# Kernel optimization log

Hardware: AMD Instinct MI355X
Metric: run time of the kernel (lower is better)

## Reference

```python
import jax, jax.numpy as jnp
import numpy as np

B, S, E = 8, 4096, 128
H, O = 64, 64  # attention_hidden_dim, out_dim


def setup_inputs() -> dict:
    key = jax.random.key(0)
    ks = jax.random.split(key, 4)
    x = jax.random.normal(ks[0], (B, S, E), dtype=jnp.float32)
    Wq = jax.random.normal(ks[1], (E, H), dtype=jnp.float32) * (1.0 / np.sqrt(E))
    Wk = jax.random.normal(ks[2], (E, H), dtype=jnp.float32) * (1.0 / np.sqrt(E))
    Wv = jax.random.normal(ks[3], (E, O), dtype=jnp.float32) * (1.0 / np.sqrt(E))
    bq = jnp.zeros((H,), dtype=jnp.float32)
    bk = jnp.zeros((H,), dtype=jnp.float32)
    bv = jnp.zeros((O,), dtype=jnp.float32)
    return {"x": x, "Wq": Wq, "bq": bq, "Wk": Wk, "bk": bk, "Wv": Wv, "bv": bv}


def reference(x, Wq, bq, Wk, bk, Wv, bv):
    # Batched version of the per-sample loop: q = x@Wq+bq, etc.
    q = jnp.einsum("bse,eh->bsh", x, Wq) + bq   # [B,S,H]
    k = jnp.einsum("bse,eh->bsh", x, Wk) + bk   # [B,S,H]
    v = jnp.einsum("bse,eo->bso", x, Wv) + bv   # [B,S,O]
    scores = jnp.einsum("bqh,bkh->bqk", q, k)   # QK^T per sample, [B,S,S]
    attn = jax.nn.softmax(scores, axis=-1)       # softmax over key dim
    out = jnp.einsum("bqk,bko->bqo", attn, v)   # [B,S,O]
    return out
```

## Files before the change

kernel.cpp:

```cpp
#include <hip/hip_runtime.h>
#include <math.h>

#define BB 8
#define SS 4096
#define EE 128
#define HH 64
#define NT 16
#define LOG2E 1.44269504088896f

typedef _Float16 f16;
typedef __attribute__((ext_vector_type(8))) _Float16 f16x8;
typedef __attribute__((ext_vector_type(4))) float f32x4;

__device__ __forceinline__ unsigned int pk2h(float a, float b) {
    return __builtin_bit_cast(unsigned int, __builtin_amdgcn_cvt_pkrtz(a, b));
}

__device__ __forceinline__ void async_copy16(void* lds, const void* g) {
    __builtin_amdgcn_global_load_lds(
        (const __attribute__((address_space(1))) void*)g,
        (__attribute__((address_space(3))) void*)lds, 16, 0, 0);
}

__device__ __forceinline__ void vm_barrier() {
    asm volatile("s_waitcnt vmcnt(0) lgkmcnt(0)" ::: "memory");
    __builtin_amdgcn_s_barrier();
    __builtin_amdgcn_sched_barrier(0);
}

__global__ __launch_bounds__(256) void wtrans_kernel(
    const float* __restrict__ Wq, const float* __restrict__ Wk,
    const float* __restrict__ Wv, f16* __restrict__ Wt)
{
    const int idx = blockIdx.x * 256 + threadIdx.x;
    if (idx >= 192 * 128) return;
    const int col = idx >> 7, e = idx & 127;
    const float v = (col < 64)  ? Wq[e * 64 + col] * LOG2E
                  : (col < 128) ? Wk[e * 64 + (col - 64)]
                                : Wv[e * 64 + (col - 128)];
    Wt[col * 128 + e] = (f16)v;
}

__global__ __launch_bounds__(256) void qkv_kernel(
    const float* __restrict__ x, const f16* __restrict__ Wt,
    const float* __restrict__ bq, const float* __restrict__ bk,
    const float* __restrict__ bv,
    f16* __restrict__ Q, f16* __restrict__ K, f16* __restrict__ Vt)
{
    __shared__ __align__(16) short xs[64 * EE];
    const int tid = threadIdx.x;
    const long rowbase = (long)blockIdx.x * 64;

    {
        const float4* xg = (const float4*)(x + rowbase * EE);
#pragma unroll
        for (int j = 0; j < 8; ++j) {
            const int eidx = tid * 32 + j * 4;
            const float4 v = xg[eidx >> 2];
            unsigned long long pk =
                (unsigned long long)pk2h(v.x, v.y) |
                ((unsigned long long)pk2h(v.z, v.w) << 32);
            const int row = eidx >> 7;
            const int off = (row * 256 + (eidx & 127) * 2) ^ ((row & 7) << 4);
            *(unsigned long long*)((char*)xs + off) = pk;
        }
    }
    __syncthreads();

    const int lane = tid & 63;
    const int wid  = tid >> 6;
    const int ln15 = lane & 15;
    const int lg   = lane >> 4;

    f16x8 xa[4];
    {
        const int row = wid * 16 + ln15;
        const int swz = (row & 7) << 4;
#pragma unroll
        for (int s = 0; s < 4; ++s)
            xa[s] = *(const f16x8*)((const char*)xs + ((row * 256 + lg * 16 + s * 64) ^ swz));
    }

    f32x4 acc[12];
#pragma unroll
    for (int ct = 0; ct < 12; ++ct) acc[ct] = (f32x4){0.f, 0.f, 0.f, 0.f};

#pragma unroll
    for (int ct = 0; ct < 12; ++ct) {
        const f16* wtp = Wt + (ct * 16 + ln15) * 128 + lg * 8;
#pragma unroll
        for (int s = 0; s < 4; ++s) {
            const f16x8 wb = *(const f16x8*)(wtp + s * 32);
            acc[ct] = __builtin_amdgcn_mfma_f32_16x16x32_f16(xa[s], wb, acc[ct], 0, 0, 0);
        }
    }

    const long grow0 = rowbase + wid * 16 + 4 * lg;
#pragma unroll
    for (int ct = 0; ct < 4; ++ct) {
        const int col = ct * 16 + ln15;
        const float b = bq[col] * LOG2E;
#pragma unroll
        for (int r = 0; r < 4; ++r)
            Q[(grow0 + r) * HH + col] = (f16)(acc[ct][r] + b);
    }
#pragma unroll
    for (int ct = 4; ct < 8; ++ct) {
        const int col = (ct - 4) * 16 + ln15;
        const float b = bk[col];
#pragma unroll
        for (int r = 0; r < 4; ++r)
            K[(grow0 + r) * HH + col] = (f16)(acc[ct][r] + b);
    }
    {
        const long batch = rowbase >> 12;
        const long inrow = (rowbase & 4095) + wid * 16 + 4 * lg;
#pragma unroll
        for (int ct = 8; ct < 12; ++ct) {
            const int o = (ct - 8) * 16 + ln15;
            const float b = bv[o];
            unsigned long long pk =
                (unsigned long long)pk2h(acc[ct][0] + b, acc[ct][1] + b) |
                ((unsigned long long)pk2h(acc[ct][2] + b, acc[ct][3] + b) << 32);
            *(unsigned long long*)(Vt + ((long)batch * HH + o) * SS + inrow) = pk;
        }
    }
}

__global__ __launch_bounds__(256, 4) void flash_kernel(
    const f16* __restrict__ Q, const f16* __restrict__ K,
    const f16* __restrict__ Vt, f16* __restrict__ Onorm,
    float* __restrict__ lse)
{
    __shared__ __align__(16) short k_s[2][64 * HH];
    __shared__ __align__(16) short v_s[2][64 * HH];
    __shared__ __align__(16) short p_s[4 * 16 * HH];

    const int tid  = threadIdx.x;
    const int lane = tid & 63;
    const int wid  = tid >> 6;
    const int ln15 = lane & 15;
    const int lg   = lane >> 4;
    const int batch = blockIdx.x & 7;
    const int rest  = blockIdx.x >> 3;
    const int split = rest & 3;
    const int qtile = rest >> 2;
    const int k0base = split * (SS / 4);

    f16x8 qf[2];
    {
        const long qrow = (long)batch * SS + qtile * 64 + wid * 16 + ln15;
        const f16* qp = Q + qrow * HH + lg * 8;
        qf[0] = *(const f16x8*)(qp);
        qf[1] = *(const f16x8*)(qp + 32);
    }

    f32x4 oacc[4];
#pragma unroll
    for (int ot = 0; ot < 4; ++ot) oacc[ot] = (f32x4){0.f, 0.f, 0.f, 0.f};
    float m = -1e30f, l = 0.f;

    short* pw = p_s + wid * (16 * HH);
    const int swq = (ln15 & 7) << 4;

    const int crow = lane >> 3;
    const int ccs  = ((lane & 7) * 16) ^ (crow << 4);
    const int row0 = wid * 16 + crow;
    const char* kgb = (const char*)(K + ((long)batch * SS + k0base) * HH);
    const char* vgb = (const char*)(Vt + (long)batch * HH * SS);
    const long koff = (long)row0 * 128 + ccs;
    const long voff = (long)row0 * (SS * 2) + k0base * 2 + ccs;

    auto issue = [&](int t, int b) __attribute__((always_inline)) {
        char* kl = (char*)k_s[b] + wid * 2048;
        char* vl = (char*)v_s[b] + wid * 2048;
        const char* kg = kgb + (long)t * (64 * 128) + koff;
        const char* vg = vgb + (long)t * 128 + voff;
        async_copy16(kl,        kg);
        async_copy16(kl + 1024, kg + 1024);
        async_copy16(vl,        vg);
        async_copy16(vl + 1024, vg + 8 * (SS * 2));
    };

    auto compute = [&](int cur) __attribute__((always_inline)) {
        const short* ks = k_s[cur];
        const short* vs = v_s[cur];

        f32x4 sacc[4];
        __builtin_amdgcn_s_setprio(1);
#pragma unroll
        for (int kt = 0; kt < 4; ++kt) {
            f32x4 a = (f32x4){0.f, 0.f, 0.f, 0.f};
            const int key = kt * 16 + ln15;
            const int rb = key * 128, swz = (key & 7) << 4;
            const f16x8 ka0 = *(const f16x8*)((const char*)ks + ((rb + lg * 16) ^ swz));
            const f16x8 ka1 = *(const f16x8*)((const char*)ks + ((rb + lg * 16 + 64) ^ swz));
            a = __builtin_amdgcn_mfma_f32_16x16x32_f16(ka0, qf[0], a, 0, 0, 0);
            a = __builtin_amdgcn_mfma_f32_16x16x32_f16(ka1, qf[1], a, 0, 0, 0);
            sacc[kt] = a;
        }
        __builtin_amdgcn_s_setprio(0);

        float t0 = fmaxf(fmaxf(sacc[0][0], sacc[0][1]), sacc[0][2]);
        float t1 = fmaxf(fmaxf(sacc[0][3], sacc[1][0]), sacc[1][1]);
        float t2 = fmaxf(fmaxf(sacc[1][2], sacc[1][3]), sacc[2][0]);
        float t3 = fmaxf(fmaxf(sacc[2][1], sacc[2][2]), sacc[2][3]);
        float t4 = fmaxf(fmaxf(sacc[3][0], sacc[3][1]), sacc[3][2]);
        float tm = fmaxf(fmaxf(fmaxf(t0, t1), t2), fmaxf(fmaxf(t3, t4), sacc[3][3]));
        tm = fmaxf(tm, __shfl_xor(tm, 16));
        tm = fmaxf(tm, __shfl_xor(tm, 32));
        if (!__all(tm <= m + 11.5f)) {
            const float mn = fmaxf(m, tm);
            const float alpha = __builtin_amdgcn_exp2f(m - mn);
            l *= alpha;
#pragma unroll
            for (int r = 0; r < 4; ++r) {
                const float ar = __shfl(alpha, lg * 4 + r);
                oacc[0][r] *= ar; oacc[1][r] *= ar;
                oacc[2][r] *= ar; oacc[3][r] *= ar;
            }
            m = mn;
        }

        float ps = 0.f;
#pragma unroll
        for (int kt = 0; kt < 4; ++kt)
#pragma unroll
            for (int r = 0; r < 4; ++r) {
                const float pv = __builtin_amdgcn_exp2f(sacc[kt][r] - m);
                sacc[kt][r] = pv;
                ps += pv;
            }
        ps += __shfl_xor(ps, 16);
        ps += __shfl_xor(ps, 32);
        l += ps;

#pragma unroll
        for (int kt = 0; kt < 4; ++kt) {
            uint2 pk;
            pk.x = pk2h(sacc[kt][0], sacc[kt][1]);
            pk.y = pk2h(sacc[kt][2], sacc[kt][3]);
            const int key = kt * 16 + lg * 4;
            *(uint2*)((char*)pw + ((ln15 * 128 + key * 2) ^ swq)) = pk;
        }

        __builtin_amdgcn_s_setprio(1);
#pragma unroll
        for (int s = 0; s < 2; ++s) {
            const f16x8 pa = *(const f16x8*)((const char*)pw + ((ln15 * 128 + lg * 16 + s * 64) ^ swq));
#pragma unroll
            for (int ot = 0; ot < 4; ++ot) {
                const int o = ot * 16 + ln15;
                const f16x8 vb = *(const f16x8*)((const char*)vs + ((o * 128 + lg * 16 + s * 64) ^ ((o & 7) << 4)));
                oacc[ot] = __builtin_amdgcn_mfma_f32_16x16x32_f16(pa, vb, oacc[ot], 0, 0, 0);
            }
        }
        __builtin_amdgcn_s_setprio(0);
    };

    issue(0, 0);
    vm_barrier();

    for (int t = 0; t < NT; t += 2) {
        issue(t + 1, 1);
        compute(0);
        vm_barrier();
        if (t + 2 < NT) issue(t + 2, 0);
        compute(1);
        vm_barrier();
    }

    const float linv = 1.0f / l;
    const long ridx = (long)split * (BB * SS) + (long)batch * SS + qtile * 64 + wid * 16;
#pragma unroll
    for (int r = 0; r < 4; ++r) {
        const float ir = __shfl(linv, lg * 4 + r);
        f16* op = Onorm + (ridx + lg * 4 + r) * HH + ln15;
        op[0]  = (f16)(oacc[0][r] * ir);
        op[16] = (f16)(oacc[1][r] * ir);
        op[32] = (f16)(oacc[2][r] * ir);
        op[48] = (f16)(oacc[3][r] * ir);
    }
    if (lg == 0)
        lse[ridx + ln15] = m + __builtin_amdgcn_logf(l);
}

__global__ __launch_bounds__(256) void merge_kernel(
    const f16* __restrict__ Onorm, const float* __restrict__ lse,
    float* __restrict__ Out)
{
    const int gid = blockIdx.x * 256 + threadIdx.x;
    const long row = gid >> 3;
    const int c0 = (gid & 7) * 8;
    const long NR = (long)BB * SS;

    float ls[4];
#pragma unroll
    for (int i = 0; i < 4; ++i) ls[i] = lse[i * NR + row];
    const float M = fmaxf(fmaxf(ls[0], ls[1]), fmaxf(ls[2], ls[3]));
    float g[4], denom = 0.f;
#pragma unroll
    for (int i = 0; i < 4; ++i) { g[i] = __builtin_amdgcn_exp2f(ls[i] - M); denom += g[i]; }
    const float inv = 1.0f / denom;

    float acc[8];
#pragma unroll
    for (int j = 0; j < 8; ++j) acc[j] = 0.f;
#pragma unroll
    for (int i = 0; i < 4; ++i) {
        const f16x8 o = *(const f16x8*)(Onorm + (i * NR + row) * HH + c0);
#pragma unroll
        for (int j = 0; j < 8; ++j) acc[j] = fmaf(g[i], (float)o[j], acc[j]);
    }
    float4 r0, r1;
    r0.x = acc[0] * inv; r0.y = acc[1] * inv; r0.z = acc[2] * inv; r0.w = acc[3] * inv;
    r1.x = acc[4] * inv; r1.y = acc[5] * inv; r1.z = acc[6] * inv; r1.w = acc[7] * inv;
    float4* dst = (float4*)(Out + row * HH + c0);
    dst[0] = r0;
    dst[1] = r1;
}

extern "C" void kernel_launch(void* const* d_in, const int* in_sizes, int n_in,
                              void* d_out, int out_size, void* d_ws, size_t ws_size,
                              hipStream_t stream) {
    const float* x  = (const float*)d_in[0];
    const float* Wq = (const float*)d_in[1];
    const float* bq = (const float*)d_in[2];
    const float* Wk = (const float*)d_in[3];
    const float* bk = (const float*)d_in[4];
    const float* Wv = (const float*)d_in[5];
    const float* bv = (const float*)d_in[6];
    float* out = (float*)d_out;

    const size_t NTOK = (size_t)BB * SS;
    f16* Q  = (f16*)d_ws;
    f16* K  = Q + NTOK * HH;
    f16* Vt = K + NTOK * HH;
    f16* Wt = Vt + NTOK * HH;
    f16* Onorm = Wt + 192 * 128;
    float* lse = (float*)(Onorm + 4 * NTOK * HH);

    wtrans_kernel<<<96, 256, 0, stream>>>(Wq, Wk, Wv, Wt);
    qkv_kernel<<<BB * SS / 64, 256, 0, stream>>>(x, Wt, bq, bk, bv, Q, K, Vt);
    flash_kernel<<<BB * 4 * (SS / 64), 256, 0, stream>>>(Q, K, Vt, Onorm, lse);
    merge_kernel<<<BB * SS * 8 / 256, 256, 0, stream>>>(Onorm, lse, out);
}
```

Measured before the change: 90.93 us.

## Switch flash attention to 32x32x16 MFMA with register-resident P and 128-query tiles

```diff
diff --git a/kernel.cpp b/kernel.cpp
--- a/kernel.cpp
+++ b/kernel.cpp
@@ -11,6 +11,8 @@
 typedef _Float16 f16;
 typedef __attribute__((ext_vector_type(8))) _Float16 f16x8;
 typedef __attribute__((ext_vector_type(4))) float f32x4;
+typedef __attribute__((ext_vector_type(16))) float f32x16;
+typedef __attribute__((ext_vector_type(4))) unsigned int u32x4;
 
 __device__ __forceinline__ unsigned int pk2h(float a, float b) {
     return __builtin_bit_cast(unsigned int, __builtin_amdgcn_cvt_pkrtz(a, b));
@@ -134,34 +136,30 @@
 {
     __shared__ __align__(16) short k_s[2][64 * HH];
     __shared__ __align__(16) short v_s[2][64 * HH];
-    __shared__ __align__(16) short p_s[4 * 16 * HH];
 
     const int tid  = threadIdx.x;
     const int lane = tid & 63;
     const int wid  = tid >> 6;
-    const int ln15 = lane & 15;
-    const int lg   = lane >> 4;
+    const int q31  = lane & 31;
+    const int h5   = lane >> 5;
     const int batch = blockIdx.x & 7;
-    const int rest  = blockIdx.x >> 3;
-    const int split = rest & 3;
-    const int qtile = rest >> 2;
+    const int split = (blockIdx.x >> 3) & 3;
+    const int qblk  = blockIdx.x >> 5;
     const int k0base = split * (SS / 4);
 
-    f16x8 qf[2];
+    f16x8 qf[4];
     {
-        const long qrow = (long)batch * SS + qtile * 64 + wid * 16 + ln15;
-        const f16* qp = Q + qrow * HH + lg * 8;
+        const long qrow = (long)batch * SS + qblk * 128 + wid * 32 + q31;
+        const f16* qp = Q + qrow * HH + 8 * h5;
         qf[0] = *(const f16x8*)(qp);
-        qf[1] = *(const f16x8*)(qp + 32);
-    }
-
-    f32x4 oacc[4];
-#pragma unroll
-    for (int ot = 0; ot < 4; ++ot) oacc[ot] = (f32x4){0.f, 0.f, 0.f, 0.f};
+        qf[1] = *(const f16x8*)(qp + 16);
+        qf[2] = *(const f16x8*)(qp + 32);
+        qf[3] = *(const f16x8*)(qp + 48);
+    }
+
+    f32x16 oacc0 = {0.f,0.f,0.f,0.f,0.f,0.f,0.f,0.f,0.f,0.f,0.f,0.f,0.f,0.f,0.f,0.f};
+    f32x16 oacc1 = oacc0;
     float m = -1e30f, l = 0.f;
-
-    short* pw = p_s + wid * (16 * HH);
-    const int swq = (ln15 & 7) << 4;
 
     const int crow = lane >> 3;
     const int ccs  = ((lane & 7) * 16) ^ (crow << 4);
@@ -183,76 +181,76 @@
     };
 
     auto compute = [&](int cur) __attribute__((always_inline)) {
-        const short* ks = k_s[cur];
-        const short* vs = v_s[cur];
-
-        f32x4 sacc[4];
+        const char* ks = (const char*)k_s[cur];
+        const char* vs = (const char*)v_s[cur];
+
+        f32x16 s0 = {0.f,0.f,0.f,0.f,0.f,0.f,0.f,0.f,0.f,0.f,0.f,0.f,0.f,0.f,0.f,0.f};
+        f32x16 s1 = s0;
         __builtin_amdgcn_s_setprio(1);
 #pragma unroll
-        for (int kt = 0; kt < 4; ++kt) {
-            f32x4 a = (f32x4){0.f, 0.f, 0.f, 0.f};
-            const int key = kt * 16 + ln15;
-            const int rb = key * 128, swz = (key & 7) << 4;
-            const f16x8 ka0 = *(const f16x8*)((const char*)ks + ((rb + lg * 16) ^ swz));
-            const f16x8 ka1 = *(const f16x8*)((const char*)ks + ((rb + lg * 16 + 64) ^ swz));
-            a = __builtin_amdgcn_mfma_f32_16x16x32_f16(ka0, qf[0], a, 0, 0, 0);
-            a = __builtin_amdgcn_mfma_f32_16x16x32_f16(ka1, qf[1], a, 0, 0, 0);
-            sacc[kt] = a;
+        for (int step = 0; step < 4; ++step) {
+            const int cb = step * 32 + 16 * h5;
+            const int r0 = q31;
+            const f16x8 ka0 = *(const f16x8*)(ks + ((r0 * 128 + cb) ^ ((r0 & 7) << 4)));
+            s0 = __builtin_amdgcn_mfma_f32_32x32x16_f16(ka0, qf[step], s0, 0, 0, 0);
+            const int r1 = q31 + 32;
+            const f16x8 ka1 = *(const f16x8*)(ks + ((r1 * 128 + cb) ^ ((r1 & 7) << 4)));
+            s1 = __builtin_amdgcn_mfma_f32_32x32x16_f16(ka1, qf[step], s1, 0, 0, 0);
         }
         __builtin_amdgcn_s_setprio(0);
 
-        float t0 = fmaxf(fmaxf(sacc[0][0], sacc[0][1]), sacc[0][2]);
-        float t1 = fmaxf(fmaxf(sacc[0][3], sacc[1][0]), sacc[1][1]);
-        float t2 = fmaxf(fmaxf(sacc[1][2], sacc[1][3]), sacc[2][0]);
-        float t3 = fmaxf(fmaxf(sacc[2][1], sacc[2][2]), sacc[2][3]);
-        float t4 = fmaxf(fmaxf(sacc[3][0], sacc[3][1]), sacc[3][2]);
-        float tm = fmaxf(fmaxf(fmaxf(t0, t1), t2), fmaxf(fmaxf(t3, t4), sacc[3][3]));
-        tm = fmaxf(tm, __shfl_xor(tm, 16));
+        float tm = s0[0];
+#pragma unroll
+        for (int i = 1; i < 16; ++i) tm = fmaxf(tm, s0[i]);
+#pragma unroll
+        for (int i = 0; i < 16; ++i) tm = fmaxf(tm, s1[i]);
         tm = fmaxf(tm, __shfl_xor(tm, 32));
         if (!__all(tm <= m + 11.5f)) {
             const float mn = fmaxf(m, tm);
             const float alpha = __builtin_amdgcn_exp2f(m - mn);
             l *= alpha;
-#pragma unroll
-            for (int r = 0; r < 4; ++r) {
-                const float ar = __shfl(alpha, lg * 4 + r);
-                oacc[0][r] *= ar; oacc[1][r] *= ar;
-                oacc[2][r] *= ar; oacc[3][r] *= ar;
-            }
+            oacc0 *= alpha;
+            oacc1 *= alpha;
             m = mn;
         }
 
+        unsigned int pk[16];
         float ps = 0.f;
 #pragma unroll
-        for (int kt = 0; kt < 4; ++kt)
-#pragma unroll
-            for (int r = 0; r < 4; ++r) {
-                const float pv = __builtin_amdgcn_exp2f(sacc[kt][r] - m);
-                sacc[kt][r] = pv;
-                ps += pv;
-            }
-        ps += __shfl_xor(ps, 16);
+        for (int i = 0; i < 8; ++i) {
+            const float a = __builtin_amdgcn_exp2f(s0[2 * i] - m);
+            const float b = __builtin_amdgcn_exp2f(s0[2 * i + 1] - m);
+            ps += a + b;
+            pk[i] = pk2h(a, b);
+        }
+#pragma unroll
+        for (int i = 0; i < 8; ++i) {
+            const float a = __builtin_amdgcn_exp2f(s1[2 * i] - m);
+            const float b = __builtin_amdgcn_exp2f(s1[2 * i + 1] - m);
+            ps += a + b;
+            pk[8 + i] = pk2h(a, b);
+        }
         ps += __shfl_xor(ps, 32);
         l += ps;
 
-#pragma unroll
-        for (int kt = 0; kt < 4; ++kt) {
-            uint2 pk;
-            pk.x = pk2h(sacc[kt][0], sacc[kt][1]);
-            pk.y = pk2h(sacc[kt][2], sacc[kt][3]);
-            const int key = kt * 16 + lg * 4;
-            *(uint2*)((char*)pw + ((ln15 * 128 + key * 2) ^ swq)) = pk;
-        }
-
         __builtin_amdgcn_s_setprio(1);
 #pragma unroll
-        for (int s = 0; s < 2; ++s) {
-            const f16x8 pa = *(const f16x8*)((const char*)pw + ((ln15 * 128 + lg * 16 + s * 64) ^ swq));
-#pragma unroll
-            for (int ot = 0; ot < 4; ++ot) {
-                const int o = ot * 16 + ln15;
-                const f16x8 vb = *(const f16x8*)((const char*)vs + ((o * 128 + lg * 16 + s * 64) ^ ((o & 7) << 4)));
-                oacc[ot] = __builtin_amdgcn_mfma_f32_16x16x32_f16(pa, vb, oacc[ot], 0, 0, 0);
+        for (int mb = 0; mb < 4; ++mb) {
+            const u32x4 pw = {pk[4 * mb], pk[4 * mb + 1], pk[4 * mb + 2], pk[4 * mb + 3]};
+            const f16x8 pb = __builtin_bit_cast(f16x8, pw);
+            const int cb_lo = 32 * mb + 8 * h5;
+#pragma unroll
+            for (int oh = 0; oh < 2; ++oh) {
+                const int row = q31 + 32 * oh;
+                const int swz = (row & 7) << 4;
+                const uint2 lo = *(const uint2*)(vs + ((row * 128 + cb_lo) ^ swz));
+                const uint2 hi = *(const uint2*)(vs + ((row * 128 + cb_lo + 16) ^ swz));
+                const u32x4 w = {lo.x, lo.y, hi.x, hi.y};
+                const f16x8 va = __builtin_bit_cast(f16x8, w);
+                if (oh == 0)
+                    oacc0 = __builtin_amdgcn_mfma_f32_32x32x16_f16(va, pb, oacc0, 0, 0, 0);
+                else
+                    oacc1 = __builtin_amdgcn_mfma_f32_32x32x16_f16(va, pb, oacc1, 0, 0, 0);
             }
         }
         __builtin_amdgcn_s_setprio(0);
@@ -271,18 +269,16 @@
     }
 
     const float linv = 1.0f / l;
-    const long ridx = (long)split * (BB * SS) + (long)batch * SS + qtile * 64 + wid * 16;
-#pragma unroll
-    for (int r = 0; r < 4; ++r) {
-        const float ir = __shfl(linv, lg * 4 + r);
-        f16* op = Onorm + (ridx + lg * 4 + r) * HH + ln15;
-        op[0]  = (f16)(oacc[0][r] * ir);
-        op[16] = (f16)(oacc[1][r] * ir);
-        op[32] = (f16)(oacc[2][r] * ir);
-        op[48] = (f16)(oacc[3][r] * ir);
-    }
-    if (lg == 0)
-        lse[ridx + ln15] = m + __builtin_amdgcn_logf(l);
+    const long tok = (long)split * (BB * SS) + (long)batch * SS + qblk * 128 + wid * 32 + q31;
+    f16* ob = Onorm + tok * HH;
+#pragma unroll
+    for (int i = 0; i < 16; ++i) {
+        const int od = (i & 3) + 8 * (i >> 2) + 4 * h5;
+        ob[od]      = (f16)(oacc0[i] * linv);
+        ob[od + 32] = (f16)(oacc1[i] * linv);
+    }
+    if (h5 == 0)
+        lse[tok] = m + __builtin_amdgcn_logf(l);
 }
 
 __global__ __launch_bounds__(256) void merge_kernel(
@@ -342,6 +338,6 @@
 
     wtrans_kernel<<<96, 256, 0, stream>>>(Wq, Wk, Wv, Wt);
     qkv_kernel<<<BB * SS / 64, 256, 0, stream>>>(x, Wt, bq, bk, bv, Q, K, Vt);
-    flash_kernel<<<BB * 4 * (SS / 64), 256, 0, stream>>>(Q, K, Vt, Onorm, lse);
+    flash_kernel<<<BB * 4 * (SS / 128), 256, 0, stream>>>(Q, K, Vt, Onorm, lse);
     merge_kernel<<<BB * SS * 8 / 256, 256, 0, stream>>>(Onorm, lse, out);
 }
```

New measurement: 81.93 us. 9.9% less time.
